# Performance work log

Measured on AMD Instinct MI355X. Metric: run time of the kernel, lower is better.

The kernel has to match this reference:

```python
import jax, jax.numpy as jnp
import numpy as np

N, E, B = 40000, 640000, 8192
IN, META, HID, OUT = 768, 6, 256, 128
NE, K, REL, NET = 4, 2, 200, 3
NL, NH, FF = 4, 4, 512


def setup_inputs():
    key = jax.random.key(0)
    keys = iter(jax.random.split(key, 64))
    def p(*shape):
        return jax.random.normal(next(keys), shape, jnp.float32) * 0.02
    return dict(
        x=jax.random.normal(next(keys), (N, IN + META), jnp.float32),
        noise=jax.random.normal(next(keys), (3, B, NE), jnp.float32),
        g_lin1_w=p(HID, IN + META), g_lin1_b=p(HID),
        conv_W=p(2, HID, HID), conv_Wr=p(2, HID, REL), conv_a=p(2, 3 * HID),
        conv_Wres=p(2, HID, HID), conv_rel=p(2, NET, REL),
        g_lin2_w=p(OUT, HID), g_lin2_b=p(OUT),
        te_w=p(OUT, IN), te_b=p(OUT),
        me_w1=p(HID, META), me_b1=p(HID), me_w2=p(OUT, HID), me_b2=p(OUT),
        moe_gate_w=p(3, NE, OUT), moe_noise_w=p(3, OUT),
        moe_w1=p(3, NE, 4 * OUT, OUT), moe_b1=p(3, NE, 4 * OUT),
        moe_w2=p(3, NE, OUT, 4 * OUT), moe_b2=p(3, NE, OUT),
        tf_qkv_w=p(NL, 3 * OUT, OUT), tf_qkv_b=p(NL, 3 * OUT),
        tf_out_w=p(NL, OUT, OUT), tf_out_b=p(NL, OUT),
        tf_ln1_g=jnp.ones((NL, OUT), jnp.float32), tf_ln1_b=jnp.zeros((NL, OUT), jnp.float32),
        tf_ff1_w=p(NL, FF, OUT), tf_ff1_b=p(NL, FF),
        tf_ff2_w=p(NL, OUT, FF), tf_ff2_b=p(NL, OUT),
        tf_ln2_g=jnp.ones((NL, OUT), jnp.float32), tf_ln2_b=jnp.zeros((NL, OUT), jnp.float32),
        clf_w=p(2, 3 * OUT), clf_b=p(2),
        edge_index=jax.random.randint(next(keys), (2, E), 0, N),
        edge_type=jax.random.randint(next(keys), (E,), 0, NET),
        batch_size=B,
    )


def _seg_softmax(logit, seg, n):
    m = jax.ops.segment_max(logit, seg, num_segments=n)
    e = jnp.exp(logit - m[seg])
    s = jax.ops.segment_sum(e, seg, num_segments=n)
    return e / (s[seg] + 1e-16)


def _hgn_layer(h, src, dst, et, W, Wr, a, Wres, rel, final):
    n, d = h.shape[0], W.shape[0]
    Wx = h @ W.T  # [N, HID]
    # a(cat(Wx_i, Wx_j, Wr_rel)) decomposed: per-node + per-edge-type scalars
    s_i = Wx @ a[:d]
    s_j = Wx @ a[d:2 * d]
    r_s = (rel @ Wr.T) @ a[2 * d:]  # [NET]
    logit = jax.nn.leaky_relu(s_i[dst] + s_j[src] + r_s[et], 0.2)
    alpha = _seg_softmax(logit, dst, n)
    agg = jax.ops.segment_sum(Wx[src] * alpha[:, None], dst, num_segments=n)
    out = jax.nn.elu(agg + h @ Wres.T)
    if final:
        out = out / jnp.maximum(jnp.linalg.norm(out, axis=1, keepdims=True), 1e-12)
    return out


def _moe(xv, eps, gate_w, noise_w, w1, b1, w2, b2):
    g = xv @ gate_w.T                       # [B, NE]
    nsd = jax.nn.softplus(xv @ noise_w)     # [B]
    h = g + eps * nsd[:, None]
    _, bot = jax.lax.top_k(-h, K)           # bottom-K experts get -inf
    drop = jnp.sum(jax.nn.one_hot(bot, NE, dtype=h.dtype), axis=1) > 0
    h = jnp.where(drop, -jnp.inf, h)
    L = jax.nn.softmax(h, axis=1)
    logits, idx = jax.lax.top_k(L, K)
    tmp = L.sum(0)
    loss = (jnp.std(tmp, ddof=1) / jnp.mean(tmp)) ** 2
    comb = jnp.einsum('bs,bse->be', logits, jax.nn.one_hot(idx, NE, dtype=L.dtype))
    h1 = jax.nn.relu(jnp.einsum('bd,ehd->ebh', xv, w1) + b1[:, None, :])
    eo = jnp.einsum('ebh,eoh->ebo', h1, w2) + b2[:, None, :]  # [NE, B, OUT]
    return jnp.einsum('be,ebo->bo', comb, eo), loss


def _ln(x, g, b):
    mu = x.mean(-1, keepdims=True)
    var = x.var(-1, keepdims=True)
    return (x - mu) / jnp.sqrt(var + 1e-5) * g + b


def _tf_layer(x, qkv_w, qkv_b, out_w, out_b, ln1g, ln1b, f1w, f1b, f2w, f2b, ln2g, ln2b):
    Bq, S, D = x.shape
    hd = D // NH
    qkv = x @ qkv_w.T + qkv_b
    q, k, v = jnp.split(qkv, 3, axis=-1)
    q = q.reshape(Bq, S, NH, hd)
    k = k.reshape(Bq, S, NH, hd)
    v = v.reshape(Bq, S, NH, hd)
    att = jax.nn.softmax(jnp.einsum('bshd,bthd->bhst', q, k) / jnp.sqrt(jnp.float32(hd)), axis=-1)
    o = jnp.einsum('bhst,bthd->bshd', att, v).reshape(Bq, S, D)
    x = _ln(x + o @ out_w.T + out_b, ln1g, ln1b)
    ff = jax.nn.relu(x @ f1w.T + f1b) @ f2w.T + f2b
    return _ln(x + ff, ln2g, ln2b)


def _forward(x, noise, g_lin1_w, g_lin1_b, conv_W, conv_Wr, conv_a, conv_Wres, conv_rel,
             g_lin2_w, g_lin2_b, te_w, te_b, me_w1, me_b1, me_w2, me_b2,
             moe_gate_w, moe_noise_w, moe_w1, moe_b1, moe_w2, moe_b2,
             tf_qkv_w, tf_qkv_b, tf_out_w, tf_out_b, tf_ln1_g, tf_ln1_b,
             tf_ff1_w, tf_ff1_b, tf_ff2_w, tf_ff2_b, tf_ln2_g, tf_ln2_b,
             clf_w, clf_b, edge_index, edge_type, batch_size):
    src, dst = edge_index[0], edge_index[1]
    # graph encoder (dropout is eval no-op)
    h = jax.nn.relu(x @ g_lin1_w.T + g_lin1_b)
    h = _hgn_layer(h, src, dst, edge_type, conv_W[0], conv_Wr[0], conv_a[0], conv_Wres[0], conv_rel[0], False)
    h = _hgn_layer(h, src, dst, edge_type, conv_W[1], conv_Wr[1], conv_a[1], conv_Wres[1], conv_rel[1], True)
    graph = jax.nn.relu(h @ g_lin2_w.T + g_lin2_b)
    x_g = graph[:batch_size]
    text = x[:batch_size, :IN]
    meta = x[:batch_size, IN:]
    x_t = jax.nn.relu(text @ te_w.T + te_b)
    x_m = jax.nn.relu(jax.nn.relu(meta @ me_w1.T + me_b1) @ me_w2.T + me_b2)
    outs, losses = [], []
    for i, xv in enumerate((x_g, x_t, x_m)):
        o, l = _moe(xv, noise[i], moe_gate_w[i], moe_noise_w[i], moe_w1[i], moe_b1[i], moe_w2[i], moe_b2[i])
        outs.append(o)
        losses.append(l)
    loss = losses[0] + losses[1] + losses[2]
    z = jnp.stack(outs, axis=1)  # [B, 3, OUT]
    for li in range(NL):
        z = _tf_layer(z, tf_qkv_w[li], tf_qkv_b[li], tf_out_w[li], tf_out_b[li],
                      tf_ln1_g[li], tf_ln1_b[li], tf_ff1_w[li], tf_ff1_b[li],
                      tf_ff2_w[li], tf_ff2_b[li], tf_ln2_g[li], tf_ln2_b[li])
    logits = z.reshape(z.shape[0], -1) @ clf_w.T + clf_b
    return logits, loss


def reference(x, noise, g_lin1_w, g_lin1_b, conv_W, conv_Wr, conv_a, conv_Wres, conv_rel,
              g_lin2_w, g_lin2_b, te_w, te_b, me_w1, me_b1, me_w2, me_b2,
              moe_gate_w, moe_noise_w, moe_w1, moe_b1, moe_w2, moe_b2,
              tf_qkv_w, tf_qkv_b, tf_out_w, tf_out_b, tf_ln1_g, tf_ln1_b,
              tf_ff1_w, tf_ff1_b, tf_ff2_w, tf_ff2_b, tf_ln2_g, tf_ln2_b,
              clf_w, clf_b, edge_index, edge_type, batch_size):
    return _forward(x, noise, g_lin1_w, g_lin1_b, conv_W, conv_Wr, conv_a, conv_Wres, conv_rel,
                    g_lin2_w, g_lin2_b, te_w, te_b, me_w1, me_b1, me_w2, me_b2,
                    moe_gate_w, moe_noise_w, moe_w1, moe_b1, moe_w2, moe_b2,
                    tf_qkv_w, tf_qkv_b, tf_out_w, tf_out_b, tf_ln1_g, tf_ln1_b,
                    tf_ff1_w, tf_ff1_b, tf_ff2_w, tf_ff2_b, tf_ln2_g, tf_ln2_b,
                    clf_w, clf_b, edge_index, edge_type, batch_size)
```

## Files before the change

kernel.cpp:

```cpp
#include <hip/hip_runtime.h>
#include <hip/hip_bf16.h>
#include <math.h>

#define NN 40000
#define EE 640000
#define BB 8192
#define IN_DIM 768
#define META_DIM 6
#define XDIM 774
#define HID 256
#define OUT_D 128
#define NEXP 4
#define NET_T 3
#define REL_D 200
#define NLAY 4
#define FF_D 512

typedef __attribute__((ext_vector_type(8))) short short8;
typedef __attribute__((ext_vector_type(4))) float f32x4;

__device__ __forceinline__ ushort f2bf(float f) {
    union { float f; unsigned u; } a; a.f = f;
    unsigned u = a.u;
    unsigned r = (u + 0x7FFFu + ((u >> 16) & 1u)) >> 16;
    return (ushort)r;
}
__device__ __forceinline__ float bf2f(ushort h) {
    union { unsigned u; float f; } a; a.u = ((unsigned)h) << 16;
    return a.f;
}

__global__ void cvt_kernel(const float* __restrict__ src, int ldsrc, int Kreal,
                           ushort* __restrict__ hi, ushort* __restrict__ lo,
                           int R, int ldp)
{
    size_t i = (size_t)blockIdx.x * blockDim.x + threadIdx.x;
    size_t total = (size_t)R * ldp;
    if (i >= total) return;
    int col = (int)(i % ldp);
    int row = (int)(i / ldp);
    float v = (col < Kreal) ? src[(size_t)row * ldsrc + col] : 0.f;
    ushort h = f2bf(v);
    float rem = v - bf2f(h);
    hi[i] = h;
    lo[i] = f2bf(rem);
}

static void cvt(const float* src, int ldsrc, int Kreal, ushort* hi, ushort* lo,
                int R, int ldp, hipStream_t s)
{
    size_t total = (size_t)R * ldp;
    cvt_kernel<<<(int)((total + 255) / 256), 256, 0, s>>>(src, ldsrc, Kreal, hi, lo, R, ldp);
}

template<int ACT, int HAS_RES, int OUT_SPLIT>
__global__ __launch_bounds__(256) void mfma3_128(
    const ushort* __restrict__ Ahi, const ushort* __restrict__ Alo, int lda,
    const ushort* __restrict__ Bhi, const ushort* __restrict__ Blo, int ldb,
    const float* __restrict__ bias, const float* __restrict__ res,
    float* __restrict__ C, ushort* __restrict__ Chi, ushort* __restrict__ Clo,
    int M, int Nn, int K)
{
    __shared__ __align__(16) ushort Ash[128 * 40];
    __shared__ __align__(16) ushort Asl[128 * 40];
    __shared__ __align__(16) ushort Bsh[128 * 40];
    __shared__ __align__(16) ushort Bsl[128 * 40];

    int bn = blockIdx.x * 128;
    int bm = blockIdx.y * 128;
    int t = threadIdx.x;
    int wave = t >> 6, lane = t & 63;
    int wm = wave & 1, wn = wave >> 1;
    int quad = lane >> 4, r = lane & 15;

    f32x4 acc[4][4];
#pragma unroll
    for (int i = 0; i < 4; i++)
#pragma unroll
        for (int j = 0; j < 4; j++) acc[i][j] = (f32x4){0.f, 0.f, 0.f, 0.f};

    for (int k0 = 0; k0 < K; k0 += 32) {
#pragma unroll
        for (int i = 0; i < 2; i++) {
            int idx = t + i * 256;
            int row = idx >> 2, c8 = idx & 3;
            int grow = bm + row; if (grow > M - 1) grow = M - 1;
            size_t off = (size_t)grow * lda + k0 + c8 * 8;
            *(short8*)&Ash[row * 40 + c8 * 8] = *(const short8*)(Ahi + off);
            *(short8*)&Asl[row * 40 + c8 * 8] = *(const short8*)(Alo + off);
        }
#pragma unroll
        for (int i = 0; i < 2; i++) {
            int idx = t + i * 256;
            int row = idx >> 2, c8 = idx & 3;
            size_t off = (size_t)(bn + row) * ldb + k0 + c8 * 8;
            *(short8*)&Bsh[row * 40 + c8 * 8] = *(const short8*)(Bhi + off);
            *(short8*)&Bsl[row * 40 + c8 * 8] = *(const short8*)(Blo + off);
        }
        __syncthreads();

        short8 ah[4], al[4], bh[4], bl[4];
#pragma unroll
        for (int i = 0; i < 4; i++) {
            int ro = (wm * 64 + i * 16 + r) * 40 + quad * 8;
            ah[i] = *(const short8*)&Ash[ro];
            al[i] = *(const short8*)&Asl[ro];
        }
#pragma unroll
        for (int j = 0; j < 4; j++) {
            int ro = (wn * 64 + j * 16 + r) * 40 + quad * 8;
            bh[j] = *(const short8*)&Bsh[ro];
            bl[j] = *(const short8*)&Bsl[ro];
        }
#pragma unroll
        for (int j = 0; j < 4; j++)
#pragma unroll
            for (int i = 0; i < 4; i++)
                acc[i][j] = __builtin_amdgcn_mfma_f32_16x16x32_bf16(ah[i], bh[j], acc[i][j], 0, 0, 0);
#pragma unroll
        for (int j = 0; j < 4; j++)
#pragma unroll
            for (int i = 0; i < 4; i++)
                acc[i][j] = __builtin_amdgcn_mfma_f32_16x16x32_bf16(ah[i], bl[j], acc[i][j], 0, 0, 0);
#pragma unroll
        for (int j = 0; j < 4; j++)
#pragma unroll
            for (int i = 0; i < 4; i++)
                acc[i][j] = __builtin_amdgcn_mfma_f32_16x16x32_bf16(al[i], bh[j], acc[i][j], 0, 0, 0);
        __syncthreads();
    }

#pragma unroll
    for (int j = 0; j < 4; j++) {
        int col = bn + wn * 64 + j * 16 + r;
        float bc = bias ? bias[col] : 0.f;
#pragma unroll
        for (int i = 0; i < 4; i++) {
#pragma unroll
            for (int reg = 0; reg < 4; reg++) {
                int row = bm + wm * 64 + i * 16 + quad * 4 + reg;
                if (row >= M) continue;
                float v = acc[i][j][reg] + bc;
                if (HAS_RES) v += res[(size_t)row * Nn + col];
                if (ACT == 1) v = fmaxf(v, 0.f);
                else if (ACT == 2) v = (v > 0.f) ? v : expm1f(v);
                if (OUT_SPLIT) {
                    ushort h = f2bf(v);
                    Chi[(size_t)row * Nn + col] = h;
                    Clo[(size_t)row * Nn + col] = f2bf(v - bf2f(h));
                } else {
                    C[(size_t)row * Nn + col] = v;
                }
            }
        }
    }
}

template<int ACT, int HAS_RES, int OUT_SPLIT>
static void m128_launch(const ushort* Ahi, const ushort* Alo, int lda,
                        const ushort* Bhi, const ushort* Blo, int ldb,
                        const float* bias, const float* res,
                        float* C, ushort* Chi, ushort* Clo,
                        int M, int Nn, int K, hipStream_t s)
{
    dim3 grid(Nn / 128, (M + 127) / 128);
    mfma3_128<ACT, HAS_RES, OUT_SPLIT><<<grid, 256, 0, s>>>(
        Ahi, Alo, lda, Bhi, Blo, ldb, bias, res, C, Chi, Clo, M, Nn, K);
}

template<int ACT>
__global__ void gemm_kernel(const float* __restrict__ A, int lda,
                            const float* __restrict__ Bw,
                            const float* __restrict__ bias,
                            const float* __restrict__ res,
                            float* __restrict__ C, int M, int Nn, int K)
{
    __shared__ float As[16][68];
    __shared__ float Bs[16][68];
    int bm = blockIdx.y * 64, bn = blockIdx.x * 64;
    int t = threadIdx.x;
    int tx = t & 15, ty = t >> 4;
    float acc[4][4] = {{0.f}};

    for (int k0 = 0; k0 < K; k0 += 16) {
#pragma unroll
        for (int i = 0; i < 4; i++) {
            int l = t * 4 + i; int mm = l >> 4, kk = l & 15;
            int gm = bm + mm, gk = k0 + kk;
            As[kk][mm] = (gm < M && gk < K) ? A[(size_t)gm * lda + gk] : 0.f;
        }
#pragma unroll
        for (int i = 0; i < 4; i++) {
            int l = t * 4 + i; int nn = l >> 4, kk = l & 15;
            int gn = bn + nn, gk = k0 + kk;
            Bs[kk][nn] = (gn < Nn && gk < K) ? Bw[(size_t)gn * K + gk] : 0.f;
        }
        __syncthreads();
#pragma unroll
        for (int kk = 0; kk < 16; kk++) {
            float4 a4 = *reinterpret_cast<const float4*>(&As[kk][ty * 4]);
            float4 b4 = *reinterpret_cast<const float4*>(&Bs[kk][tx * 4]);
            float a0[4] = {a4.x, a4.y, a4.z, a4.w};
            float b0[4] = {b4.x, b4.y, b4.z, b4.w};
#pragma unroll
            for (int i = 0; i < 4; i++)
#pragma unroll
                for (int j = 0; j < 4; j++)
                    acc[i][j] += a0[i] * b0[j];
        }
        __syncthreads();
    }
#pragma unroll
    for (int i = 0; i < 4; i++) {
        int gm = bm + ty * 4 + i; if (gm >= M) continue;
#pragma unroll
        for (int j = 0; j < 4; j++) {
            int gn = bn + tx * 4 + j; if (gn >= Nn) continue;
            float v = acc[i][j];
            if (bias) v += bias[gn];
            if (res)  v += res[(size_t)gm * Nn + gn];
            if (ACT == 1) v = fmaxf(v, 0.f);
            else if (ACT == 2) v = (v > 0.f) ? v : expm1f(v);
            C[(size_t)gm * Nn + gn] = v;
        }
    }
}

static void launch_gemm(int act, const float* A, int lda, const float* Bw,
                        const float* bias, const float* res, float* C,
                        int M, int Nn, int K, hipStream_t s)
{
    dim3 grid((Nn + 63) / 64, (M + 63) / 64);
    dim3 blk(256);
    if (act == 0)      gemm_kernel<0><<<grid, blk, 0, s>>>(A, lda, Bw, bias, res, C, M, Nn, K);
    else if (act == 1) gemm_kernel<1><<<grid, blk, 0, s>>>(A, lda, Bw, bias, res, C, M, Nn, K);
    else               gemm_kernel<2><<<grid, blk, 0, s>>>(A, lda, Bw, bias, res, C, M, Nn, K);
}

template<int ACT, int A_BF16, int OUT_BF16>
__global__ __launch_bounds__(256) void mfma_gemm(
    const void* __restrict__ Ap, size_t strideAz,
    const float* __restrict__ Bw, size_t strideBz,
    const float* __restrict__ bias, size_t strideBiasz,
    void* __restrict__ Cp, size_t strideCz,
    int M, int Nn, int K)
{
    __shared__ __align__(16) ushort As[128 * 40];
    __shared__ __align__(16) ushort Bs[64 * 40];

    int z = blockIdx.z;
    const float*  Af  = (const float*)Ap  + (A_BF16 ? 0 : z * strideAz);
    const ushort* Ab  = (const ushort*)Ap + (A_BF16 ? z * strideAz : 0);
    const float*  Bwz = Bw + z * strideBz;
    const float*  bz  = bias ? bias + z * strideBiasz : nullptr;
    float*  Cf = (float*)Cp  + (OUT_BF16 ? 0 : z * strideCz);
    ushort* Cb = (ushort*)Cp + (OUT_BF16 ? z * strideCz : 0);

    int bn = blockIdx.x * 64;
    int bm = blockIdx.y * 128;
    int t = threadIdx.x;
    int wave = t >> 6, lane = t & 63;
    int wm = wave & 1, wn = wave >> 1;
    int quad = lane >> 4, r = lane & 15;

    f32x4 acc[4][2];
#pragma unroll
    for (int i = 0; i < 4; i++)
#pragma unroll
        for (int j = 0; j < 2; j++) acc[i][j] = (f32x4){0.f, 0.f, 0.f, 0.f};

    for (int k0 = 0; k0 < K; k0 += 32) {
        if (A_BF16) {
#pragma unroll
            for (int i = 0; i < 2; i++) {
                int idx = t + i * 256;
                int row = idx >> 2, c8 = idx & 3;
                short8 v = *(const short8*)(Ab + (size_t)(bm + row) * K + k0 + c8 * 8);
                *(short8*)&As[row * 40 + c8 * 8] = v;
            }
        } else {
#pragma unroll
            for (int i = 0; i < 4; i++) {
                int idx = t + i * 256;
                int row = idx >> 3, c4 = idx & 7;
                float4 f = *(const float4*)(Af + (size_t)(bm + row) * K + k0 + c4 * 4);
                ushort4 u; u.x = f2bf(f.x); u.y = f2bf(f.y); u.z = f2bf(f.z); u.w = f2bf(f.w);
                *(ushort4*)&As[row * 40 + c4 * 4] = u;
            }
        }
#pragma unroll
        for (int i = 0; i < 2; i++) {
            int idx = t + i * 256;
            int row = idx >> 3, c4 = idx & 7;
            float4 f = *(const float4*)(Bwz + (size_t)(bn + row) * K + k0 + c4 * 4);
            ushort4 u; u.x = f2bf(f.x); u.y = f2bf(f.y); u.z = f2bf(f.z); u.w = f2bf(f.w);
            *(ushort4*)&Bs[row * 40 + c4 * 4] = u;
        }
        __syncthreads();

        short8 af[4], bf[2];
#pragma unroll
        for (int i = 0; i < 4; i++)
            af[i] = *(const short8*)&As[(wm * 64 + i * 16 + r) * 40 + quad * 8];
#pragma unroll
        for (int j = 0; j < 2; j++)
            bf[j] = *(const short8*)&Bs[(wn * 32 + j * 16 + r) * 40 + quad * 8];
#pragma unroll
        for (int i = 0; i < 4; i++)
#pragma unroll
            for (int j = 0; j < 2; j++)
                acc[i][j] = __builtin_amdgcn_mfma_f32_16x16x32_bf16(af[i], bf[j], acc[i][j], 0, 0, 0);
        __syncthreads();
    }

    float bcol[2];
#pragma unroll
    for (int j = 0; j < 2; j++)
        bcol[j] = bz ? bz[bn + wn * 32 + j * 16 + r] : 0.f;
#pragma unroll
    for (int i = 0; i < 4; i++) {
#pragma unroll
        for (int j = 0; j < 2; j++) {
            int col = bn + wn * 32 + j * 16 + r;
#pragma unroll
            for (int reg = 0; reg < 4; reg++) {
                int row = bm + wm * 64 + i * 16 + quad * 4 + reg;
                float v = acc[i][j][reg] + bcol[j];
                if (ACT == 1) v = fmaxf(v, 0.f);
                if (OUT_BF16) Cb[(size_t)row * Nn + col] = f2bf(v);
                else          Cf[(size_t)row * Nn + col] = v;
            }
        }
    }
}

template<int ACT, int A_BF16, int OUT_BF16>
static void mfma_launch(const void* A, size_t sAz, const float* Bw, size_t sBz,
                        const float* bias, size_t sbz, void* C, size_t sCz,
                        int M, int Nn, int K, int batch, hipStream_t s)
{
    dim3 grid(Nn / 64, M / 128, batch);
    mfma_gemm<ACT, A_BF16, OUT_BF16><<<grid, 256, 0, s>>>(A, sAz, Bw, sBz, bias, sbz, C, sCz, M, Nn, K);
}

// ... 8 lines not shown
    for (int i = 0; i < 4; i++) {
        float xv = r[l + 64 * i];
        v1 += xv * a[l + 64 * i];
        v2 += xv * a[HID + l + 64 * i];
    }
    for (int off = 32; off; off >>= 1) { v1 += __shfl_down(v1, off); v2 += __shfl_down(v2, off); }
    if (l == 0) { s_i[m] = v1; s_j[m] = v2; }
}

__global__ void rs_kernel(const float* __restrict__ Wr, const float* __restrict__ rel,
                          const float* __restrict__ a3, float* __restrict__ rs)
{
    __shared__ float red[256];
    int tt = blockIdx.x; int j = threadIdx.x;
    const float* relr = rel + tt * REL_D;
    const float* wr = Wr + (size_t)j * REL_D;
    float wsum = 0.f;
    for (int k = 0; k < REL_D; k++) wsum += wr[k] * relr[k];
    red[j] = wsum * a3[j];
    __syncthreads();
    for (int s2 = 128; s2; s2 >>= 1) { if (j < s2) red[j] += red[j + s2]; __syncthreads(); }
    if (j == 0) rs[tt] = red[0];
}

__global__ void deg_kernel(const int* __restrict__ dst, int* __restrict__ deg)
{
    int e = blockIdx.x * blockDim.x + threadIdx.x;
    if (e < EE) atomicAdd(&deg[dst[e]], 1);
}

__global__ void scan_kernel(const int* __restrict__ deg, int* __restrict__ rowstart,
                            int* __restrict__ cursor, int n)
{
    __shared__ int buf[1024];
    __shared__ int carry;
    int t = threadIdx.x;
    if (t == 0) carry = 0;
    __syncthreads();
    for (int c = 0; c < n; c += 1024) {
        int v = (c + t < n) ? deg[c + t] : 0;
        buf[t] = v;
        __syncthreads();
        for (int off = 1; off < 1024; off <<= 1) {
            int x = (t >= off) ? buf[t - off] : 0;
            __syncthreads();
            buf[t] += x;
            __syncthreads();
        }
        int incl = buf[t];
        int base = carry;
        if (c + t < n) { rowstart[c + t] = base + incl - v; cursor[c + t] = base + incl - v; }
        __syncthreads();
        if (t == 1023) carry = base + incl;
        __syncthreads();
    }
    if (t == 0) rowstart[n] = carry;
}

__global__ void fill_kernel(const int* __restrict__ src, const int* __restrict__ dst,
                            const int* __restrict__ et, int* __restrict__ cursor,
                            unsigned* __restrict__ csr_val)
{
    int e = blockIdx.x * blockDim.x + threadIdx.x;
    if (e >= EE) return;
    int d = dst[e];
    int pos = atomicAdd(&cursor[d], 1);
    csr_val[pos] = (unsigned)src[e] | ((unsigned)et[e] << 16);
}

__global__ void csr_agg_kernel(const unsigned* __restrict__ csr_val,
                               const int* __restrict__ rowstart,
                               const float* __restrict__ s_i, const float* __restrict__ s_j,
                               const float* __restrict__ rsv,
                               const float* __restrict__ Wx, float* __restrict__ agg)
{
    int t = threadIdx.x; int w = t >> 6, l = t & 63;
    int node = blockIdx.x * 4 + w; if (node >= NN) return;
    int start = rowstart[node], end = rowstart[node + 1];
    float r0 = rsv[0], r1 = rsv[1], r2 = rsv[2];
    float si = s_i[node];

    float m = -INFINITY;
    for (int i = start + l; i < end; i += 64) {
        unsigned v = csr_val[i];
        int s = v & 0xFFFF; int et = v >> 16;
        float rr = (et == 0) ? r0 : ((et == 1) ? r1 : r2);
        float lg = si + s_j[s] + rr;
        lg = (lg >= 0.f) ? lg : 0.2f * lg;
        m = fmaxf(m, lg);
    }
    for (int off = 32; off; off >>= 1) m = fmaxf(m, __shfl_down(m, off));
    m = __shfl(m, 0);

    float a0 = 0.f, a1 = 0.f, a2 = 0.f, a3 = 0.f, ssum = 0.f;
    for (int c = start; c < end; c += 64) {
        int nchunk = min(64, end - c);
        float wgt = 0.f; int sidx = 0;
        if (l < nchunk) {
            unsigned v = csr_val[c + l];
            sidx = v & 0xFFFF; int et = v >> 16;
            float rr = (et == 0) ? r0 : ((et == 1) ? r1 : r2);
            float lg = si + s_j[sidx] + rr;
            lg = (lg >= 0.f) ? lg : 0.2f * lg;
            wgt = expf(lg - m);
            ssum += wgt;
        }
        for (int j = 0; j < nchunk; j++) {
            float wj = __shfl(wgt, j);
            int sj = __shfl(sidx, j);
            const float* wr = Wx + (size_t)sj * HID;
            a0 += wj * wr[l];
            a1 += wj * wr[l + 64];
            a2 += wj * wr[l + 128];
            a3 += wj * wr[l + 192];
        }
    }
    for (int off = 32; off; off >>= 1) ssum += __shfl_down(ssum, off);
    ssum = __shfl(ssum, 0);
    float inv = 1.f / (ssum + 1e-16f);
    float* ar = agg + (size_t)node * HID;
    ar[l] = a0 * inv; ar[l + 64] = a1 * inv; ar[l + 128] = a2 * inv; ar[l + 192] = a3 * inv;
}

__global__ void rownorm_split(ushort* __restrict__ hi, ushort* __restrict__ lo, int n)
{
    int t = threadIdx.x; int w = t >> 6, l = t & 63;
    int m = blockIdx.x * 4 + w; if (m >= n) return;
    size_t base = (size_t)m * HID;
    float vals[4]; float q = 0.f;
#pragma unroll
    for (int i = 0; i < 4; i++) {
        vals[i] = bf2f(hi[base + l + 64 * i]) + bf2f(lo[base + l + 64 * i]);
        q += vals[i] * vals[i];
    }
    for (int off = 32; off; off >>= 1) q += __shfl_down(q, off);
    q = __shfl(q, 0);
    float inv = 1.f / fmaxf(sqrtf(q), 1e-12f);
#pragma unroll
    for (int i = 0; i < 4; i++) {
        float nv = vals[i] * inv;
        ushort h = f2bf(nv);
        hi[base + l + 64 * i] = h;
        lo[base + l + 64 * i] = f2bf(nv - bf2f(h));
    }
}

__global__ void moe_gate_kernel(const float* __restrict__ xv, const float* __restrict__ gate_w,
                                const float* __restrict__ noise_w, const float* __restrict__ eps,
                                float* __restrict__ comb, float* __restrict__ tmpsum)
{
    __shared__ float part[4];
    int t = threadIdx.x; int w = t >> 6, l = t & 63;
    if (t < 4) part[t] = 0.f;
    __syncthreads();
    int b = blockIdx.x * 4 + w;
    const float* xr = xv + (size_t)b * OUT_D;
    float x0 = xr[l], x1 = xr[l + 64];
    float dots[5];
#pragma unroll
    for (int e = 0; e < 4; e++) {
        const float* gw = gate_w + e * OUT_D;
        float v = x0 * gw[l] + x1 * gw[l + 64];
        for (int off = 32; off; off >>= 1) v += __shfl_down(v, off);
        dots[e] = v;
    }
    {
        float v = x0 * noise_w[l] + x1 * noise_w[l + 64];
        for (int off = 32; off; off >>= 1) v += __shfl_down(v, off);
        dots[4] = v;
    }
    if (l == 0) {
        float xg = dots[4];
        float nsd = (xg > 20.f) ? xg : log1pf(expf(xg));
        float hv[4];
#pragma unroll
        for (int e = 0; e < 4; e++) hv[e] = dots[e] + eps[(size_t)b * 4 + e] * nsd;
        int i1 = 0;
// ... 142 lines not shown
    const float* me_b2     = (const float*)d_in[16];
    const float* moe_gate_w  = (const float*)d_in[17];
    const float* moe_noise_w = (const float*)d_in[18];
    const float* moe_w1    = (const float*)d_in[19];
    const float* moe_b1    = (const float*)d_in[20];
    const float* moe_w2    = (const float*)d_in[21];
    const float* moe_b2    = (const float*)d_in[22];
    const float* tf_qkv_w  = (const float*)d_in[23];
    const float* tf_qkv_b  = (const float*)d_in[24];
    const float* tf_out_w  = (const float*)d_in[25];
    const float* tf_out_b  = (const float*)d_in[26];
    const float* tf_ln1_g  = (const float*)d_in[27];
    const float* tf_ln1_b  = (const float*)d_in[28];
    const float* tf_ff1_w  = (const float*)d_in[29];
    const float* tf_ff1_b  = (const float*)d_in[30];
    const float* tf_ff2_w  = (const float*)d_in[31];
    const float* tf_ff2_b  = (const float*)d_in[32];
    const float* tf_ln2_g  = (const float*)d_in[33];
    const float* tf_ln2_b  = (const float*)d_in[34];
    const float* clf_w     = (const float*)d_in[35];
    const float* clf_b     = (const float*)d_in[36];
    const int*   edge_index = (const int*)d_in[37];
    const int*   edge_type  = (const int*)d_in[38];

    float* ws = (float*)d_ws;

    const size_t F_A = 0;
    const size_t F_B = 10240000;
    const size_t F_C = 22822912;
    const size_t F_D = 33062912;
    const size_t F_M = 43302912;
    const size_t F_X = 44200000;

    ushort* hAhi  = (ushort*)(ws + F_A);
    ushort* hAlo  = (ushort*)(ws + F_A + 5120000);
    float* qkv    = ws + F_A;
    float* wx     = ws + F_B;
    float* graph  = ws + F_B;
    ushort* ff1bf = (ushort*)(ws + F_B);
    float* agg    = ws + F_C;
    float* x_mh   = ws + F_C;
    ushort* h1bf  = (ushort*)(ws + F_C);
    float* attn_o = ws + F_C;
    float* tmp1   = ws + F_C + 3200000;
    ushort* hBhi  = (ushort*)(ws + F_D);
    ushort* hBlo  = (ushort*)(ws + F_D + 5120000);
    float* z      = ws + F_D;
    float* x_t    = ws + F_D + 3200000;
    float* x_m    = ws + F_D + 4300000;
    float* eo     = ws + F_D + 5400000;

    float* s_i    = ws + F_M;
    float* s_j    = ws + F_M + 40000;
    float* rsv    = ws + F_M + 80000;
    float* comb   = ws + F_M + 80016;
    float* tmpsum = ws + F_M + 112784;
    int* deg      = (int*)(ws + F_M + 120000);
    int* rowstart = (int*)(ws + F_M + 161000);
    int* cursor   = (int*)(ws + F_M + 202000);
    unsigned* csr_val = (unsigned*)(ws + F_M + 242000);

    ushort* xhi  = (ushort*)(ws + F_X);
    ushort* xlo  = (ushort*)(ws + F_X + 16000000);
    ushort* wbh  = (ushort*)(ws + F_X + 32000000);
    ushort* wbl  = (ushort*)(ws + F_X + 32110000);
    ushort* mhhi = (ushort*)(ws + F_X + 32220000);
    ushort* mhlo = (ushort*)(ws + F_X + 33280000);

    const int* srcv = edge_index;
    const int* dstv = edge_index + EE;

    hipMemsetAsync(deg, 0, NN * sizeof(int), stream);
    deg_kernel<<<(EE + 255) / 256, 256, 0, stream>>>(dstv, deg);
    scan_kernel<<<1, 1024, 0, stream>>>(deg, rowstart, cursor, NN);
    fill_kernel<<<(EE + 255) / 256, 256, 0, stream>>>(srcv, dstv, edge_type, cursor, csr_val);

    cvt(x, XDIM, XDIM, xhi, xlo, NN, 800, stream);
    cvt(g_lin1_w, XDIM, XDIM, wbh, wbl, HID, 800, stream);
    m128_launch<1, 0, 1>(xhi, xlo, 800, wbh, wbl, 800, g_lin1_b, nullptr,
                         nullptr, hAhi, hAlo, NN, HID, 800, stream);

    ushort *inhi = hAhi, *inlo = hAlo, *outhi = hBhi, *outlo = hBlo;
    for (int layer = 0; layer < 2; layer++) {
        const float* W    = conv_W    + (size_t)layer * HID * HID;
        const float* Wr   = conv_Wr   + (size_t)layer * HID * REL_D;
        const float* a    = conv_a    + (size_t)layer * 3 * HID;
        const float* Wres = conv_Wres + (size_t)layer * HID * HID;
        const float* rel  = conv_rel  + (size_t)layer * NET_T * REL_D;

        cvt(W, HID, HID, wbh, wbl, HID, HID, stream);
        m128_launch<0, 0, 0>(inhi, inlo, HID, wbh, wbl, HID, nullptr, nullptr,
                             wx, nullptr, nullptr, NN, HID, HID, stream);
        sisj_kernel<<<NN / 4, 256, 0, stream>>>(wx, a, s_i, s_j, NN);
        rs_kernel<<<NET_T, 256, 0, stream>>>(Wr, rel, a + 2 * HID, rsv);
        csr_agg_kernel<<<NN / 4, 256, 0, stream>>>(csr_val, rowstart, s_i, s_j, rsv, wx, agg);
        cvt(Wres, HID, HID, wbh, wbl, HID, HID, stream);
        m128_launch<2, 1, 1>(inhi, inlo, HID, wbh, wbl, HID, nullptr, agg,
                             nullptr, outhi, outlo, NN, HID, HID, stream);
        ushort* th = inhi; inhi = outhi; outhi = th;
        ushort* tl = inlo; inlo = outlo; outlo = tl;
    }
    rownorm_split<<<NN / 4, 256, 0, stream>>>(inhi, inlo, NN);

    cvt(g_lin2_w, HID, HID, wbh, wbl, OUT_D, HID, stream);
    m128_launch<1, 0, 0>(inhi, inlo, HID, wbh, wbl, HID, g_lin2_b, nullptr,
                         graph, nullptr, nullptr, NN, OUT_D, HID, stream);

    cvt(te_w, IN_DIM, IN_DIM, wbh, wbl, OUT_D, IN_DIM, stream);
    m128_launch<1, 0, 0>(xhi, xlo, 800, wbh, wbl, IN_DIM, te_b, nullptr,
                         x_t, nullptr, nullptr, BB, OUT_D, IN_DIM, stream);
    launch_gemm(1, x + IN_DIM, XDIM, me_w1, me_b1, nullptr, x_mh, BB, HID, META_DIM, stream);
    cvt(x_mh, HID, HID, mhhi, mhlo, BB, HID, stream);
    cvt(me_w2, HID, HID, wbh, wbl, OUT_D, HID, stream);
    m128_launch<1, 0, 0>(mhhi, mhlo, HID, wbh, wbl, HID, me_b2, nullptr,
                         x_m, nullptr, nullptr, BB, OUT_D, HID, stream);

    hipMemsetAsync(tmpsum, 0, 16 * sizeof(float), stream);
    const float* xvs[3] = { graph, x_t, x_m };
    for (int v = 0; v < 3; v++) {
        const float* xv = xvs[v];
        moe_gate_kernel<<<BB / 4, 256, 0, stream>>>(
            xv, moe_gate_w + (size_t)v * NEXP * OUT_D, moe_noise_w + (size_t)v * OUT_D,
            noise + (size_t)v * BB * NEXP, comb, tmpsum + v * 4);
        mfma_launch<1, 0, 1>(xv, 0,
                             moe_w1 + (size_t)v * 4 * FF_D * OUT_D, (size_t)FF_D * OUT_D,
                             moe_b1 + (size_t)v * 4 * FF_D, FF_D,
                             h1bf, (size_t)BB * FF_D,
                             BB, FF_D, OUT_D, 4, stream);
        mfma_launch<0, 1, 0>(h1bf, (size_t)BB * FF_D,
                             moe_w2 + (size_t)v * 4 * OUT_D * FF_D, (size_t)OUT_D * FF_D,
                             moe_b2 + (size_t)v * 4 * OUT_D, OUT_D,
                             eo, (size_t)BB * OUT_D,
                             BB, OUT_D, FF_D, 4, stream);
        moe_combine_kernel<<<(BB * OUT_D) / 256, 256, 0, stream>>>(eo, comb, z + v * OUT_D);
    }

    const int MT = BB * 3;
    for (int li = 0; li < NLAY; li++) {
        mfma_launch<0, 0, 0>(z, 0, tf_qkv_w + (size_t)li * 384 * 128, 0,
                             tf_qkv_b + li * 384, 0, qkv, 0, MT, 384, 128, 1, stream);
        attn_kernel<<<(BB * 4) / 8, 256, 0, stream>>>(qkv, attn_o);
        mfma_launch<0, 0, 0>(attn_o, 0, tf_out_w + (size_t)li * 128 * 128, 0,
                             tf_out_b + li * 128, 0, tmp1, 0, MT, 128, 128, 1, stream);
        ln_residual_kernel<<<MT / 4, 256, 0, stream>>>(z, tmp1, tf_ln1_g + li * 128, tf_ln1_b + li * 128, MT);
        mfma_launch<1, 0, 1>(z, 0, tf_ff1_w + (size_t)li * 512 * 128, 0,
                             tf_ff1_b + li * 512, 0, ff1bf, 0, MT, 512, 128, 1, stream);
        mfma_launch<0, 1, 0>(ff1bf, 0, tf_ff2_w + (size_t)li * 128 * 512, 0,
                             tf_ff2_b + li * 128, 0, tmp1, 0, MT, 128, 512, 1, stream);
// ... 7 lines not shown
```

Baseline: 1.877 ms.

## Pack bf16 hi/lo splits, prefetch GEMM tiles, parallelize scan, unroll CSR gather

The split-bf16 hi/lo arrays are interleaved into one packed 32-bit word per element, so each GEMM operand is read with a single stream. Weight matrices are now split inside the GEMM from fp32 rather than by separate conversion kernels. Both MFMA GEMMs gain register prefetch of the next K tile to overlap global loads with compute. The single-block scan becomes a two-level per-thread scan, and the CSR aggregation gather is unrolled by four to put more loads in flight. The trade-off is more register pressure and redundant per-block conversion of the weights.

```diff
diff --git a/kernel.cpp b/kernel.cpp
--- a/kernel.cpp
+++ b/kernel.cpp
@@ -29,10 +29,14 @@
     union { unsigned u; float f; } a; a.u = ((unsigned)h) << 16;
     return a.f;
 }
-
-__global__ void cvt_kernel(const float* __restrict__ src, int ldsrc, int Kreal,
-                           ushort* __restrict__ hi, ushort* __restrict__ lo,
-                           int R, int ldp)
+__device__ __forceinline__ unsigned packsplit(float v) {
+    ushort h = f2bf(v);
+    ushort lo = f2bf(v - bf2f(h));
+    return ((unsigned)h << 16) | lo;
+}
+
+__global__ void cvt_pack_kernel(const float* __restrict__ src, int ldsrc, int Kreal,
+                                unsigned* __restrict__ pk, int R, int ldp)
 {
     size_t i = (size_t)blockIdx.x * blockDim.x + threadIdx.x;
     size_t total = (size_t)R * ldp;
@@ -40,31 +44,31 @@
     int col = (int)(i % ldp);
     int row = (int)(i / ldp);
     float v = (col < Kreal) ? src[(size_t)row * ldsrc + col] : 0.f;
-    ushort h = f2bf(v);
-    float rem = v - bf2f(h);
-    hi[i] = h;
-    lo[i] = f2bf(rem);
-}
-
-static void cvt(const float* src, int ldsrc, int Kreal, ushort* hi, ushort* lo,
-                int R, int ldp, hipStream_t s)
+    pk[i] = packsplit(v);
+}
+
+static void cvt_pack(const float* src, int ldsrc, int Kreal, unsigned* pk,
+                     int R, int ldp, hipStream_t s)
 {
     size_t total = (size_t)R * ldp;
-    cvt_kernel<<<(int)((total + 255) / 256), 256, 0, s>>>(src, ldsrc, Kreal, hi, lo, R, ldp);
-}
-
-template<int ACT, int HAS_RES, int OUT_SPLIT>
+    cvt_pack_kernel<<<(int)((total + 255) / 256), 256, 0, s>>>(src, ldsrc, Kreal, pk, R, ldp);
+}
+
+template<int ACT, int HAS_RES, int OUT_SPLIT, int B_PACKED>
 __global__ __launch_bounds__(256) void mfma3_128(
-    const ushort* __restrict__ Ahi, const ushort* __restrict__ Alo, int lda,
-    const ushort* __restrict__ Bhi, const ushort* __restrict__ Blo, int ldb,
+    const unsigned* __restrict__ Ap, int lda,
+    const void* __restrict__ Bp, int ldb,
     const float* __restrict__ bias, const float* __restrict__ res,
-    float* __restrict__ C, ushort* __restrict__ Chi, ushort* __restrict__ Clo,
+    float* __restrict__ C, unsigned* __restrict__ Cpk,
     int M, int Nn, int K)
 {
     __shared__ __align__(16) ushort Ash[128 * 40];
     __shared__ __align__(16) ushort Asl[128 * 40];
     __shared__ __align__(16) ushort Bsh[128 * 40];
     __shared__ __align__(16) ushort Bsl[128 * 40];
+
+    const float*    Bf = (const float*)Bp;
+    const unsigned* Bk = (const unsigned*)Bp;
 
     int bn = blockIdx.x * 128;
     int bm = blockIdx.y * 128;
@@ -73,33 +77,83 @@
     int wm = wave & 1, wn = wave >> 1;
     int quad = lane >> 4, r = lane & 15;
 
+    int arow0 = t >> 2,           ac80 = t & 3;
+    int arow1 = (t + 256) >> 2,   ac81 = t & 3;
+
+    uint4 apre[2][2];
+    uint4 bprek[2][2];
+    float4 bpref[2][2];
+
+    auto loadA = [&](int k0) {
+        int g0 = bm + arow0; if (g0 > M - 1) g0 = M - 1;
+        int g1 = bm + arow1; if (g1 > M - 1) g1 = M - 1;
+        const unsigned* p0 = Ap + (size_t)g0 * lda + k0 + ac80 * 8;
+        const unsigned* p1 = Ap + (size_t)g1 * lda + k0 + ac81 * 8;
+        apre[0][0] = *(const uint4*)p0; apre[0][1] = *(const uint4*)(p0 + 4);
+        apre[1][0] = *(const uint4*)p1; apre[1][1] = *(const uint4*)(p1 + 4);
+    };
+    auto loadB = [&](int k0) {
+        if (B_PACKED) {
+            const unsigned* p0 = Bk + (size_t)(bn + arow0) * ldb + k0 + ac80 * 8;
+            const unsigned* p1 = Bk + (size_t)(bn + arow1) * ldb + k0 + ac81 * 8;
+            bprek[0][0] = *(const uint4*)p0; bprek[0][1] = *(const uint4*)(p0 + 4);
+            bprek[1][0] = *(const uint4*)p1; bprek[1][1] = *(const uint4*)(p1 + 4);
+        } else {
+            const float* p0 = Bf + (size_t)(bn + arow0) * ldb + k0 + ac80 * 8;
+            const float* p1 = Bf + (size_t)(bn + arow1) * ldb + k0 + ac81 * 8;
+            bpref[0][0] = *(const float4*)p0; bpref[0][1] = *(const float4*)(p0 + 4);
+            bpref[1][0] = *(const float4*)p1; bpref[1][1] = *(const float4*)(p1 + 4);
+        }
+    };
+    auto storeTiles = [&]() {
+#pragma unroll
+        for (int i = 0; i < 2; i++) {
+            int row = i ? arow1 : arow0, c8 = i ? ac81 : ac80;
+            unsigned u[8] = {apre[i][0].x, apre[i][0].y, apre[i][0].z, apre[i][0].w,
+                             apre[i][1].x, apre[i][1].y, apre[i][1].z, apre[i][1].w};
+            short8 hi, lo;
+#pragma unroll
+            for (int e = 0; e < 8; e++) { hi[e] = (short)(u[e] >> 16); lo[e] = (short)(u[e] & 0xFFFFu); }
+            *(short8*)&Ash[row * 40 + c8 * 8] = hi;
+            *(short8*)&Asl[row * 40 + c8 * 8] = lo;
+        }
+#pragma unroll
+        for (int i = 0; i < 2; i++) {
+            int row = i ? arow1 : arow0, c8 = i ? ac81 : ac80;
+            short8 hi, lo;
+            if (B_PACKED) {
+                unsigned u[8] = {bprek[i][0].x, bprek[i][0].y, bprek[i][0].z, bprek[i][0].w,
+                                 bprek[i][1].x, bprek[i][1].y, bprek[i][1].z, bprek[i][1].w};
+#pragma unroll
+                for (int e = 0; e < 8; e++) { hi[e] = (short)(u[e] >> 16); lo[e] = (short)(u[e] & 0xFFFFu); }
+            } else {
+                float f[8] = {bpref[i][0].x, bpref[i][0].y, bpref[i][0].z, bpref[i][0].w,
+                              bpref[i][1].x, bpref[i][1].y, bpref[i][1].z, bpref[i][1].w};
+#pragma unroll
+                for (int e = 0; e < 8; e++) {
+                    ushort h = f2bf(f[e]);
+                    hi[e] = (short)h;
+                    lo[e] = (short)f2bf(f[e] - bf2f(h));
+                }
+            }
+            *(short8*)&Bsh[row * 40 + c8 * 8] = hi;
+            *(short8*)&Bsl[row * 40 + c8 * 8] = lo;
+        }
+    };
+
     f32x4 acc[4][4];
 #pragma unroll
     for (int i = 0; i < 4; i++)
 #pragma unroll
         for (int j = 0; j < 4; j++) acc[i][j] = (f32x4){0.f, 0.f, 0.f, 0.f};
 
+    loadA(0); loadB(0);
     for (int k0 = 0; k0 < K; k0 += 32) {
-#pragma unroll
-        for (int i = 0; i < 2; i++) {
-            int idx = t + i * 256;
-            int row = idx >> 2, c8 = idx & 3;
-            int grow = bm + row; if (grow > M - 1) grow = M - 1;
-            size_t off = (size_t)grow * lda + k0 + c8 * 8;
-            *(short8*)&Ash[row * 40 + c8 * 8] = *(const short8*)(Ahi + off);
-            *(short8*)&Asl[row * 40 + c8 * 8] = *(const short8*)(Alo + off);
-        }
-#pragma unroll
-        for (int i = 0; i < 2; i++) {
-            int idx = t + i * 256;
-            int row = idx >> 2, c8 = idx & 3;
-            size_t off = (size_t)(bn + row) * ldb + k0 + c8 * 8;
-            *(short8*)&Bsh[row * 40 + c8 * 8] = *(const short8*)(Bhi + off);
-            *(short8*)&Bsl[row * 40 + c8 * 8] = *(const short8*)(Blo + off);
-        }
+        storeTiles();
         __syncthreads();
-
-        short8 ah[4], al[4], bh[4], bl[4];
+        if (k0 + 32 < K) { loadA(k0 + 32); loadB(k0 + 32); }
+
+        short8 ah[4], al[4];
 #pragma unroll
         for (int i = 0; i < 4; i++) {
             int ro = (wm * 64 + i * 16 + r) * 40 + quad * 8;
@@ -109,24 +163,18 @@
 #pragma unroll
         for (int j = 0; j < 4; j++) {
             int ro = (wn * 64 + j * 16 + r) * 40 + quad * 8;
-            bh[j] = *(const short8*)&Bsh[ro];
-            bl[j] = *(const short8*)&Bsl[ro];
-        }
-#pragma unroll
-        for (int j = 0; j < 4; j++)
+            short8 bh = *(const short8*)&Bsh[ro];
+            short8 bl = *(const short8*)&Bsl[ro];
 #pragma unroll
             for (int i = 0; i < 4; i++)
-                acc[i][j] = __builtin_amdgcn_mfma_f32_16x16x32_bf16(ah[i], bh[j], acc[i][j], 0, 0, 0);
-#pragma unroll
-        for (int j = 0; j < 4; j++)
+                acc[i][j] = __builtin_amdgcn_mfma_f32_16x16x32_bf16(ah[i], bh, acc[i][j], 0, 0, 0);
 #pragma unroll
             for (int i = 0; i < 4; i++)
-                acc[i][j] = __builtin_amdgcn_mfma_f32_16x16x32_bf16(ah[i], bl[j], acc[i][j], 0, 0, 0);
-#pragma unroll
-        for (int j = 0; j < 4; j++)
+                acc[i][j] = __builtin_amdgcn_mfma_f32_16x16x32_bf16(ah[i], bl, acc[i][j], 0, 0, 0);
 #pragma unroll
             for (int i = 0; i < 4; i++)
-                acc[i][j] = __builtin_amdgcn_mfma_f32_16x16x32_bf16(al[i], bh[j], acc[i][j], 0, 0, 0);
+                acc[i][j] = __builtin_amdgcn_mfma_f32_16x16x32_bf16(al[i], bh, acc[i][j], 0, 0, 0);
+        }
         __syncthreads();
     }
 
@@ -144,28 +192,22 @@
                 if (HAS_RES) v += res[(size_t)row * Nn + col];
                 if (ACT == 1) v = fmaxf(v, 0.f);
                 else if (ACT == 2) v = (v > 0.f) ? v : expm1f(v);
-                if (OUT_SPLIT) {
-                    ushort h = f2bf(v);
-                    Chi[(size_t)row * Nn + col] = h;
-                    Clo[(size_t)row * Nn + col] = f2bf(v - bf2f(h));
-                } else {
-                    C[(size_t)row * Nn + col] = v;
-                }
+                if (OUT_SPLIT) Cpk[(size_t)row * Nn + col] = packsplit(v);
+                else           C[(size_t)row * Nn + col] = v;
             }
         }
     }
 }
 
-template<int ACT, int HAS_RES, int OUT_SPLIT>
-static void m128_launch(const ushort* Ahi, const ushort* Alo, int lda,
-                        const ushort* Bhi, const ushort* Blo, int ldb,
+template<int ACT, int HAS_RES, int OUT_SPLIT, int B_PACKED>
+static void m128_launch(const unsigned* Ap, int lda, const void* Bp, int ldb,
                         const float* bias, const float* res,
-                        float* C, ushort* Chi, ushort* Clo,
+                        float* C, unsigned* Cpk,
                         int M, int Nn, int K, hipStream_t s)
 {
     dim3 grid(Nn / 128, (M + 127) / 128);
-    mfma3_128<ACT, HAS_RES, OUT_SPLIT><<<grid, 256, 0, s>>>(
-        Ahi, Alo, lda, Bhi, Blo, ldb, bias, res, C, Chi, Clo, M, Nn, K);
+    mfma3_128<ACT, HAS_RES, OUT_SPLIT, B_PACKED><<<grid, 256, 0, s>>>(
+        Ap, lda, Bp, ldb, bias, res, C, Cpk, M, Nn, K);
 }
 
 template<int ACT>
@@ -231,10 +273,8 @@
                         int M, int Nn, int K, hipStream_t s)
 {
     dim3 grid((Nn + 63) / 64, (M + 63) / 64);
-    dim3 blk(256);
-    if (act == 0)      gemm_kernel<0><<<grid, blk, 0, s>>>(A, lda, Bw, bias, res, C, M, Nn, K);
-    else if (act == 1) gemm_kernel<1><<<grid, blk, 0, s>>>(A, lda, Bw, bias, res, C, M, Nn, K);
-    else               gemm_kernel<2><<<grid, blk, 0, s>>>(A, lda, Bw, bias, res, C, M, Nn, K);
+    if (act == 1) gemm_kernel<1><<<grid, 256, 0, s>>>(A, lda, Bw, bias, res, C, M, Nn, K);
+    else          gemm_kernel<0><<<grid, 256, 0, s>>>(A, lda, Bw, bias, res, C, M, Nn, K);
 }
 
 template<int ACT, int A_BF16, int OUT_BF16>
@@ -263,53 +303,80 @@
     int wm = wave & 1, wn = wave >> 1;
     int quad = lane >> 4, r = lane & 15;
 
-    f32x4 acc[4][2];
-#pragma unroll
-    for (int i = 0; i < 4; i++)
-#pragma unroll
-        for (int j = 0; j < 2; j++) acc[i][j] = (f32x4){0.f, 0.f, 0.f, 0.f};
-
-    for (int k0 = 0; k0 < K; k0 += 32) {
+    int ar0 = t >> 2, ac0 = t & 3;
+    int ar1 = (t + 256) >> 2;
+    int br = t >> 2, bc = t & 3;
+
+    short8 apre_b[2];
+    float4 apre_f[4];
+    float4 bpre[2];
+
+    auto loadA = [&](int k0) {
         if (A_BF16) {
-#pragma unroll
-            for (int i = 0; i < 2; i++) {
-                int idx = t + i * 256;
-                int row = idx >> 2, c8 = idx & 3;
-                short8 v = *(const short8*)(Ab + (size_t)(bm + row) * K + k0 + c8 * 8);
-                *(short8*)&As[row * 40 + c8 * 8] = v;
-            }
+            apre_b[0] = *(const short8*)(Ab + (size_t)(bm + ar0) * K + k0 + ac0 * 8);
+            apre_b[1] = *(const short8*)(Ab + (size_t)(bm + ar1) * K + k0 + ac0 * 8);
         } else {
 #pragma unroll
             for (int i = 0; i < 4; i++) {
                 int idx = t + i * 256;
                 int row = idx >> 3, c4 = idx & 7;
-                float4 f = *(const float4*)(Af + (size_t)(bm + row) * K + k0 + c4 * 4);
-                ushort4 u; u.x = f2bf(f.x); u.y = f2bf(f.y); u.z = f2bf(f.z); u.w = f2bf(f.w);
+                apre_f[i] = *(const float4*)(Af + (size_t)(bm + row) * K + k0 + c4 * 4);
+            }
+        }
+    };
+    auto loadB = [&](int k0) {
+        const float* p = Bwz + (size_t)(bn + br) * K + k0 + bc * 8;
+        bpre[0] = *(const float4*)p;
+        bpre[1] = *(const float4*)(p + 4);
+    };
+    auto storeTiles = [&]() {
+        if (A_BF16) {
+            *(short8*)&As[ar0 * 40 + ac0 * 8] = apre_b[0];
+            *(short8*)&As[ar1 * 40 + ac0 * 8] = apre_b[1];
+        } else {
+#pragma unroll
+            for (int i = 0; i < 4; i++) {
+                int idx = t + i * 256;
+                int row = idx >> 3, c4 = idx & 7;
+                ushort4 u;
+                u.x = f2bf(apre_f[i].x); u.y = f2bf(apre_f[i].y);
+                u.z = f2bf(apre_f[i].z); u.w = f2bf(apre_f[i].w);
                 *(ushort4*)&As[row * 40 + c4 * 4] = u;
             }
         }
-#pragma unroll
-        for (int i = 0; i < 2; i++) {
-            int idx = t + i * 256;
-            int row = idx >> 3, c4 = idx & 7;
-            float4 f = *(const float4*)(Bwz + (size_t)(bn + row) * K + k0 + c4 * 4);
-            ushort4 u; u.x = f2bf(f.x); u.y = f2bf(f.y); u.z = f2bf(f.z); u.w = f2bf(f.w);
-            *(ushort4*)&Bs[row * 40 + c4 * 4] = u;
-        }
+        {
+            float f[8] = {bpre[0].x, bpre[0].y, bpre[0].z, bpre[0].w,
+                          bpre[1].x, bpre[1].y, bpre[1].z, bpre[1].w};
+            short8 hb;
+#pragma unroll
+            for (int e = 0; e < 8; e++) hb[e] = (short)f2bf(f[e]);
+            *(short8*)&Bs[br * 40 + bc * 8] = hb;
+        }
+    };
+
+    f32x4 acc[4][2];
+#pragma unroll
+    for (int i = 0; i < 4; i++)
+#pragma unroll
+        for (int j = 0; j < 2; j++) acc[i][j] = (f32x4){0.f, 0.f, 0.f, 0.f};
+
+    loadA(0); loadB(0);
+    for (int k0 = 0; k0 < K; k0 += 32) {
+        storeTiles();
         __syncthreads();
-
-        short8 af[4], bf[2];
+        if (k0 + 32 < K) { loadA(k0 + 32); loadB(k0 + 32); }
+
+        short8 af[4];
 #pragma unroll
         for (int i = 0; i < 4; i++)
             af[i] = *(const short8*)&As[(wm * 64 + i * 16 + r) * 40 + quad * 8];
 #pragma unroll
-        for (int j = 0; j < 2; j++)
-            bf[j] = *(const short8*)&Bs[(wn * 32 + j * 16 + r) * 40 + quad * 8];
-#pragma unroll
-        for (int i = 0; i < 4; i++)
-#pragma unroll
-            for (int j = 0; j < 2; j++)
-                acc[i][j] = __builtin_amdgcn_mfma_f32_16x16x32_bf16(af[i], bf[j], acc[i][j], 0, 0, 0);
+        for (int j = 0; j < 2; j++) {
+            short8 bf = *(const short8*)&Bs[(wn * 32 + j * 16 + r) * 40 + quad * 8];
+#pragma unroll
+            for (int i = 0; i < 4; i++)
+                acc[i][j] = __builtin_amdgcn_mfma_f32_16x16x32_bf16(af[i], bf, acc[i][j], 0, 0, 0);
+        }
         __syncthreads();
     }
 
@@ -384,29 +451,30 @@
 __global__ void scan_kernel(const int* __restrict__ deg, int* __restrict__ rowstart,
                             int* __restrict__ cursor, int n)
 {
-    __shared__ int buf[1024];
-    __shared__ int carry;
+    __shared__ int bs[1024];
     int t = threadIdx.x;
-    if (t == 0) carry = 0;
+    int base = t * 40;
+    int loc[40];
+    int sum = 0;
+#pragma unroll
+    for (int i = 0; i < 40; i++) {
+        int v = (base + i < n) ? deg[base + i] : 0;
+        loc[i] = sum; sum += v;
+    }
+    bs[t] = sum;
     __syncthreads();
-    for (int c = 0; c < n; c += 1024) {
-        int v = (c + t < n) ? deg[c + t] : 0;
-        buf[t] = v;
+    for (int off = 1; off < 1024; off <<= 1) {
+        int x = (t >= off) ? bs[t - off] : 0;
         __syncthreads();
-        for (int off = 1; off < 1024; off <<= 1) {
-            int x = (t >= off) ? buf[t - off] : 0;
-            __syncthreads();
-            buf[t] += x;
-            __syncthreads();
-        }
-        int incl = buf[t];
-        int base = carry;
-        if (c + t < n) { rowstart[c + t] = base + incl - v; cursor[c + t] = base + incl - v; }
+        bs[t] += x;
         __syncthreads();
-        if (t == 1023) carry = base + incl;
-        __syncthreads();
-    }
-    if (t == 0) rowstart[n] = carry;
+    }
+    int excl = bs[t] - sum;
+#pragma unroll
+    for (int i = 0; i < 40; i++) {
+        if (base + i < n) { int v = excl + loc[i]; rowstart[base + i] = v; cursor[base + i] = v; }
+    }
+    if (t == 1023) rowstart[n] = bs[1023];
 }
 
 __global__ void fill_kernel(const int* __restrict__ src, const int* __restrict__ dst,
@@ -457,14 +525,33 @@
             wgt = expf(lg - m);
             ssum += wgt;
         }
-        for (int j = 0; j < nchunk; j++) {
+        int j = 0;
+        for (; j + 4 <= nchunk; j += 4) {
+            float w0 = __shfl(wgt, j),     w1 = __shfl(wgt, j + 1);
+            float w2 = __shfl(wgt, j + 2), w3 = __shfl(wgt, j + 3);
+            int s0 = __shfl(sidx, j),     s1 = __shfl(sidx, j + 1);
+            int s2 = __shfl(sidx, j + 2), s3 = __shfl(sidx, j + 3);
+            const float* p0 = Wx + (size_t)s0 * HID + l;
+            const float* p1 = Wx + (size_t)s1 * HID + l;
+            const float* p2 = Wx + (size_t)s2 * HID + l;
+            const float* p3 = Wx + (size_t)s3 * HID + l;
+            float v00 = p0[0], v01 = p0[64], v02 = p0[128], v03 = p0[192];
+            float v10 = p1[0], v11 = p1[64], v12 = p1[128], v13 = p1[192];
+            float v20 = p2[0], v21 = p2[64], v22 = p2[128], v23 = p2[192];
+            float v30 = p3[0], v31 = p3[64], v32 = p3[128], v33 = p3[192];
+            a0 += w0 * v00 + w1 * v10 + w2 * v20 + w3 * v30;
+            a1 += w0 * v01 + w1 * v11 + w2 * v21 + w3 * v31;
+            a2 += w0 * v02 + w1 * v12 + w2 * v22 + w3 * v32;
+            a3 += w0 * v03 + w1 * v13 + w2 * v23 + w3 * v33;
+        }
+        for (; j < nchunk; j++) {
             float wj = __shfl(wgt, j);
             int sj = __shfl(sidx, j);
-            const float* wr = Wx + (size_t)sj * HID;
-            a0 += wj * wr[l];
-            a1 += wj * wr[l + 64];
-            a2 += wj * wr[l + 128];
-            a3 += wj * wr[l + 192];
+            const float* wr = Wx + (size_t)sj * HID + l;
+            a0 += wj * wr[0];
+            a1 += wj * wr[64];
+            a2 += wj * wr[128];
+            a3 += wj * wr[192];
         }
     }
     for (int off = 32; off; off >>= 1) ssum += __shfl_down(ssum, off);
@@ -474,7 +561,7 @@
     ar[l] = a0 * inv; ar[l + 64] = a1 * inv; ar[l + 128] = a2 * inv; ar[l + 192] = a3 * inv;
 }
 
-__global__ void rownorm_split(ushort* __restrict__ hi, ushort* __restrict__ lo, int n)
+__global__ void rownorm_pack(unsigned* __restrict__ pk, int n)
 {
     int t = threadIdx.x; int w = t >> 6, l = t & 63;
     int m = blockIdx.x * 4 + w; if (m >= n) return;
@@ -482,19 +569,16 @@
     float vals[4]; float q = 0.f;
 #pragma unroll
     for (int i = 0; i < 4; i++) {
-        vals[i] = bf2f(hi[base + l + 64 * i]) + bf2f(lo[base + l + 64 * i]);
+        unsigned u = pk[base + l + 64 * i];
+        vals[i] = bf2f((ushort)(u >> 16)) + bf2f((ushort)(u & 0xFFFFu));
         q += vals[i] * vals[i];
     }
     for (int off = 32; off; off >>= 1) q += __shfl_down(q, off);
     q = __shfl(q, 0);
     float inv = 1.f / fmaxf(sqrtf(q), 1e-12f);
 #pragma unroll
-    for (int i = 0; i < 4; i++) {
-        float nv = vals[i] * inv;
-        ushort h = f2bf(nv);
-        hi[base + l + 64 * i] = h;
-        lo[base + l + 64 * i] = f2bf(nv - bf2f(h));
-    }
+    for (int i = 0; i < 4; i++)
+        pk[base + l + 64 * i] = packsplit(vals[i] * inv);
 }
 
 __global__ void moe_gate_kernel(const float* __restrict__ xv, const float* __restrict__ gate_w,
@@ -703,8 +787,7 @@
     const size_t F_M = 43302912;
     const size_t F_X = 44200000;
 
-    ushort* hAhi  = (ushort*)(ws + F_A);
-    ushort* hAlo  = (ushort*)(ws + F_A + 5120000);
+    unsigned* hApk = (unsigned*)(ws + F_A);
     float* qkv    = ws + F_A;
     float* wx     = ws + F_B;
     float* graph  = ws + F_B;
@@ -714,8 +797,7 @@
     ushort* h1bf  = (ushort*)(ws + F_C);
     float* attn_o = ws + F_C;
     float* tmp1   = ws + F_C + 3200000;
-    ushort* hBhi  = (ushort*)(ws + F_D);
-    ushort* hBlo  = (ushort*)(ws + F_D + 5120000);
+    unsigned* hBpk = (unsigned*)(ws + F_D);
     float* z      = ws + F_D;
     float* x_t    = ws + F_D + 3200000;
     float* x_m    = ws + F_D + 4300000;
@@ -731,12 +813,9 @@
     int* cursor   = (int*)(ws + F_M + 202000);
     unsigned* csr_val = (unsigned*)(ws + F_M + 242000);
 
-    ushort* xhi  = (ushort*)(ws + F_X);
-    ushort* xlo  = (ushort*)(ws + F_X + 16000000);
-    ushort* wbh  = (ushort*)(ws + F_X + 32000000);
-    ushort* wbl  = (ushort*)(ws + F_X + 32110000);
-    ushort* mhhi = (ushort*)(ws + F_X + 32220000);
-    ushort* mhlo = (ushort*)(ws + F_X + 33280000);
+    unsigned* xpk  = (unsigned*)(ws + F_X);
+    unsigned* wpk  = (unsigned*)(ws + F_X + 32000000);
+    unsigned* mhpk = (unsigned*)(ws + F_X + 32300000);
 
     const int* srcv = edge_index;
     const int* dstv = edge_index + EE;
@@ -746,12 +825,12 @@
     scan_kernel<<<1, 1024, 0, stream>>>(deg, rowstart, cursor, NN);
     fill_kernel<<<(EE + 255) / 256, 256, 0, stream>>>(srcv, dstv, edge_type, cursor, csr_val);
 
-    cvt(x, XDIM, XDIM, xhi, xlo, NN, 800, stream);
-    cvt(g_lin1_w, XDIM, XDIM, wbh, wbl, HID, 800, stream);
-    m128_launch<1, 0, 1>(xhi, xlo, 800, wbh, wbl, 800, g_lin1_b, nullptr,
-                         nullptr, hAhi, hAlo, NN, HID, 800, stream);
-
-    ushort *inhi = hAhi, *inlo = hAlo, *outhi = hBhi, *outlo = hBlo;
+    cvt_pack(x, XDIM, XDIM, xpk, NN, 800, stream);
+    cvt_pack(g_lin1_w, XDIM, XDIM, wpk, HID, 800, stream);
+    m128_launch<1, 0, 1, 1>(xpk, 800, wpk, 800, g_lin1_b, nullptr,
+                            nullptr, hApk, NN, HID, 800, stream);
+
+    unsigned *inpk = hApk, *outpk = hBpk;
     for (int layer = 0; layer < 2; layer++) {
         const float* W    = conv_W    + (size_t)layer * HID * HID;
         const float* Wr   = conv_Wr   + (size_t)layer * HID * REL_D;
@@ -759,32 +838,26 @@
         const float* Wres = conv_Wres + (size_t)layer * HID * HID;
         const float* rel  = conv_rel  + (size_t)layer * NET_T * REL_D;
 
-        cvt(W, HID, HID, wbh, wbl, HID, HID, stream);
-        m128_launch<0, 0, 0>(inhi, inlo, HID, wbh, wbl, HID, nullptr, nullptr,
-                             wx, nullptr, nullptr, NN, HID, HID, stream);
+        m128_launch<0, 0, 0, 0>(inpk, HID, W, HID, nullptr, nullptr,
+                                wx, nullptr, NN, HID, HID, stream);
         sisj_kernel<<<NN / 4, 256, 0, stream>>>(wx, a, s_i, s_j, NN);
         rs_kernel<<<NET_T, 256, 0, stream>>>(Wr, rel, a + 2 * HID, rsv);
         csr_agg_kernel<<<NN / 4, 256, 0, stream>>>(csr_val, rowstart, s_i, s_j, rsv, wx, agg);
-        cvt(Wres, HID, HID, wbh, wbl, HID, HID, stream);
-        m128_launch<2, 1, 1>(inhi, inlo, HID, wbh, wbl, HID, nullptr, agg,
-                             nullptr, outhi, outlo, NN, HID, HID, stream);
-        ushort* th = inhi; inhi = outhi; outhi = th;
-        ushort* tl = inlo; inlo = outlo; outlo = tl;
-    }
-    rownorm_split<<<NN / 4, 256, 0, stream>>>(inhi, inlo, NN);
-
-    cvt(g_lin2_w, HID, HID, wbh, wbl, OUT_D, HID, stream);
-    m128_launch<1, 0, 0>(inhi, inlo, HID, wbh, wbl, HID, g_lin2_b, nullptr,
-                         graph, nullptr, nullptr, NN, OUT_D, HID, stream);
-
-    cvt(te_w, IN_DIM, IN_DIM, wbh, wbl, OUT_D, IN_DIM, stream);
-    m128_launch<1, 0, 0>(xhi, xlo, 800, wbh, wbl, IN_DIM, te_b, nullptr,
-                         x_t, nullptr, nullptr, BB, OUT_D, IN_DIM, stream);
+        m128_launch<2, 1, 1, 0>(inpk, HID, Wres, HID, nullptr, agg,
+                                nullptr, outpk, NN, HID, HID, stream);
+        unsigned* tp = inpk; inpk = outpk; outpk = tp;
+    }
+    rownorm_pack<<<NN / 4, 256, 0, stream>>>(inpk, NN);
+
+    m128_launch<1, 0, 0, 0>(inpk, HID, g_lin2_w, HID, g_lin2_b, nullptr,
+                            graph, nullptr, NN, OUT_D, HID, stream);
+
+    m128_launch<1, 0, 0, 0>(xpk, 800, te_w, IN_DIM, te_b, nullptr,
+                            x_t, nullptr, BB, OUT_D, IN_DIM, stream);
     launch_gemm(1, x + IN_DIM, XDIM, me_w1, me_b1, nullptr, x_mh, BB, HID, META_DIM, stream);
-    cvt(x_mh, HID, HID, mhhi, mhlo, BB, HID, stream);
-    cvt(me_w2, HID, HID, wbh, wbl, OUT_D, HID, stream);
-    m128_launch<1, 0, 0>(mhhi, mhlo, HID, wbh, wbl, HID, me_b2, nullptr,
-                         x_m, nullptr, nullptr, BB, OUT_D, HID, stream);
+    cvt_pack(x_mh, HID, HID, mhpk, BB, HID, stream);
+    m128_launch<1, 0, 0, 0>(mhpk, HID, me_w2, HID, me_b2, nullptr,
+                            x_m, nullptr, BB, OUT_D, HID, stream);
 
     hipMemsetAsync(tmpsum, 0, 16 * sizeof(float), stream);
     const float* xvs[3] = { graph, x_t, x_m };
```

Measured after the change: 1.719 ms. -8.4%, faster.
